# Optimization experiments

Measured on AMD Instinct MI355X. Metric: run time of the kernel, lower is better.

Reference implementation:

```python
import jax, jax.numpy as jnp
import numpy as np

B, S, D, H = 4, 1024, 1024, 16
DK = D // H
EPS = 1e-6

def setup_inputs() -> dict:
    key = jax.random.key(0)
    ks = jax.random.split(key, 7)
    scale = 1.0 / np.sqrt(D)
    return {
        "query": jax.random.normal(ks[0], (B, S, D), jnp.float32),
        "key": jax.random.normal(ks[1], (B, S, D), jnp.float32),
        "value": jax.random.normal(ks[2], (B, S, D), jnp.float32),
        "Wq": jax.random.normal(ks[3], (D, D), jnp.float32) * scale,
        "Wk": jax.random.normal(ks[4], (D, D), jnp.float32) * scale,
        "Wv": jax.random.normal(ks[5], (D, D), jnp.float32) * scale,
        "Wo": jax.random.normal(ks[6], (D, D), jnp.float32) * scale,
        "ln_gamma": jnp.ones((D,), jnp.float32),
        "ln_beta": jnp.zeros((D,), jnp.float32),
    }

def reference(query, key, value, Wq, Wk, Wv, Wo, ln_gamma, ln_beta):
    residual = query
    # projections (torch Linear: x @ W.T); reshape to [B,H,S,DK]
    def proj(x, W):
        y = jnp.einsum('bsd,ed->bse', x, W)
        return y.reshape(B, S, H, DK).transpose(0, 2, 1, 3)
    q, k, v = proj(query, Wq), proj(key, Wk), proj(value, Wv)
    scores = jnp.einsum('bhqd,bhkd->bhqk', q, k) / jnp.sqrt(jnp.float32(DK))
    p = jax.nn.softmax(scores, axis=-1)
    x = jnp.einsum('bhqk,bhkd->bhqd', p, v)
    x = x.transpose(0, 2, 1, 3).reshape(B, S, D)
    x = jnp.einsum('bsd,ed->bse', x, Wo)
    x = x + residual
    mu = jnp.mean(x, axis=-1, keepdims=True)
    var = jnp.var(x, axis=-1, keepdims=True)
    x = (x - mu) / jnp.sqrt(var + EPS) * ln_gamma + ln_beta
    return x
```

## Files before the change

kernel.cpp:

```cpp
#include <hip/hip_runtime.h>
#include <hip/hip_bf16.h>

#define B_ 4
#define S_ 1024
#define D_ 1024
#define H_ 16
#define DK_ 64
#define MROWS (B_*S_)

typedef short bf16x8 __attribute__((ext_vector_type(8)));
typedef float f32x4 __attribute__((ext_vector_type(4)));
typedef unsigned short u16;
typedef unsigned u32;
typedef u16 u16x4 __attribute__((ext_vector_type(4)));

__device__ __forceinline__ u16 f2bf(float f) {
    union { float f; unsigned u; } v; v.f = f;
    unsigned u = v.u;
    u += 0x7fff + ((u >> 16) & 1);
    return (u16)(u >> 16);
}

__device__ __forceinline__ void gld_lds16(const u16* gp, u16* lp) {
    __builtin_amdgcn_global_load_lds(
        (const __attribute__((address_space(1))) void*)gp,
        (__attribute__((address_space(3))) void*)lp,
        16, 0, 0);
}

__global__ __launch_bounds__(256) void pack_bf16(
    const float* __restrict__ q, const float* __restrict__ k, const float* __restrict__ v,
    const float* __restrict__ wq, const float* __restrict__ wk,
    const float* __restrict__ wv, const float* __restrict__ wo,
    u16* __restrict__ act_dst, u16* __restrict__ w_dst)
{
    const int NACT = 3 * MROWS * D_;
    const int NW   = 4 * D_ * D_;
    for (int c = blockIdx.x * blockDim.x + threadIdx.x;
         c < (NACT + NW) / 4; c += gridDim.x * blockDim.x) {
        int e = c * 4;
        const float* s; u16* d;
        if (e < NACT) {
            int t = e >> 22;
            int off = e & (4194304 - 1);
            s = (t == 0 ? q : t == 1 ? k : v) + off;
            d = act_dst + e;
        } else {
            int e2 = e - NACT;
            int t = e2 >> 20;
            int off = e2 & (1048576 - 1);
            s = (t == 0 ? wq : t == 1 ? wk : t == 2 ? wv : wo) + off;
            d = w_dst + e2;
        }
        float4 tv = *(const float4*)s;
        u16x4 o; o[0]=f2bf(tv.x); o[1]=f2bf(tv.y); o[2]=f2bf(tv.z); o[3]=f2bf(tv.w);
        *(u16x4*)d = o;
    }
}

template<int BM, bool EPI_RESID, bool VT>
__global__ __launch_bounds__(256) void gemm_fast(
    const u16* __restrict__ Ab, const u16* __restrict__ Wb,
    u16* __restrict__ Cb, float* __restrict__ Cf, const float* __restrict__ resid)
{
    constexpr int WN = (BM == 128) ? 2 : 4;
    constexpr int WCOLS = 128 / WN;
    constexpr int NR = WCOLS / 16;
    __shared__ u16 ldsA[BM * 64];
    __shared__ u16 ldsB[128 * 64];

    const int gx = gridDim.x, gy = gridDim.y, gz = gridDim.z;
    const int nwg = gx * gy * gz;
    const int flat = blockIdx.x + gx * (blockIdx.y + gy * blockIdx.z);
    const int f = (flat & 7) * (nwg >> 3) + (flat >> 3);
    const int bx = f % gx;
    const int rem = f / gx;
    const int by = rem % gy;
    const int z = rem / gy;

    Ab += (size_t)z * MROWS * D_;
    Wb += (size_t)z * D_ * D_;
    const u16* CbT = Cb + (EPI_RESID ? 0 : (size_t)z * MROWS * D_);
    u16* Cbz = (u16*)CbT;

    const int tid = threadIdx.x, lane = tid & 63, wid = tid >> 6;
    const int wr = (BM == 128) ? (wid >> 1) : 0;
    const int wc = (BM == 128) ? (wid & 1) : wid;
    const int m0 = by * BM, n0 = bx * 128;
    const int wbase = wid * 64;

    f32x4 acc[4][NR] = {};

    for (int kt = 0; kt < 1024; kt += 64) {
        __syncthreads();
        #pragma unroll
        for (int j = 0; j < BM / 32; ++j) {
            int ch = j * 256 + tid;
            int row = ch >> 3, c8 = (ch & 7) ^ (row & 7);
            gld_lds16(Ab + (size_t)(m0 + row) * 1024 + kt + c8 * 8,
                      &ldsA[(j * 256 + wbase) * 8]);
        }
        #pragma unroll
        for (int j = 0; j < 4; ++j) {
            int ch = j * 256 + tid;
            int row = ch >> 3, c8 = (ch & 7) ^ (row & 7);
            gld_lds16(Wb + (size_t)(n0 + row) * 1024 + kt + c8 * 8,
                      &ldsB[(j * 256 + wbase) * 8]);
        }
        __syncthreads();

        #pragma unroll
        for (int ks = 0; ks < 2; ++ks) {
            const int cb = ks * 32 + (lane >> 4) * 8;
            bf16x8 af[4], bfr[NR];
            #pragma unroll
            for (int m = 0; m < 4; ++m) {
                int row = wr * 64 + m * 16 + (lane & 15);
                af[m] = *(const bf16x8*)(&ldsA[row * 64 + (cb ^ ((row & 7) << 3))]);
            }
            #pragma unroll
            for (int n = 0; n < NR; ++n) {
                int row = wc * WCOLS + n * 16 + (lane & 15);
                bfr[n] = *(const bf16x8*)(&ldsB[row * 64 + (cb ^ ((row & 7) << 3))]);
            }
            #pragma unroll
            for (int m = 0; m < 4; ++m)
                #pragma unroll
                for (int n = 0; n < NR; ++n)
                    acc[m][n] = __builtin_amdgcn_mfma_f32_16x16x32_bf16(
                        af[m], bfr[n], acc[m][n], 0, 0, 0);
        }
    }

    if (VT && z == 2) {
        #pragma unroll
        for (int m = 0; m < 4; ++m)
            #pragma unroll
            for (int n = 0; n < NR; ++n) {
                u16x4 o;
                #pragma unroll
                for (int r = 0; r < 4; ++r) o[r] = f2bf(acc[m][n][r]);
                int grow = m0 + wr * 64 + m * 16 + (lane >> 4) * 4;
                int gcol = n0 + wc * WCOLS + n * 16 + (lane & 15);
                *(u16x4*)(&Cbz[(size_t)gcol * MROWS + grow]) = o;
            }
    } else {
        #pragma unroll
        for (int m = 0; m < 4; ++m)
            #pragma unroll
            for (int n = 0; n < NR; ++n)
                #pragma unroll
                for (int r = 0; r < 4; ++r) {
                    int grow = m0 + wr * 64 + m * 16 + (lane >> 4) * 4 + r;
                    int gcol = n0 + wc * WCOLS + n * 16 + (lane & 15);
                    if (EPI_RESID)
                        Cf[(size_t)grow * 1024 + gcol] = acc[m][n][r] + resid[(size_t)grow * 1024 + gcol];
                    else
                        Cbz[(size_t)grow * 1024 + gcol] = f2bf(acc[m][n][r]);
                }
    }
}

template<bool A_BF16, bool EPI_RESID>
__global__ __launch_bounds__(256) void gemm_bt(
    const void* __restrict__ Av, const float* __restrict__ Bw,
    u16* __restrict__ Cb, float* __restrict__ Cf,
    const float* __restrict__ resid, int M, int N, int K)
{
    __shared__ u16 lds[2][128 * 64];
    const int tid  = threadIdx.x;
    const int lane = tid & 63;
    const int wid  = tid >> 6;
    const int wr = wid >> 1, wc = wid & 1;
    const int m0 = blockIdx.y * 128, n0 = blockIdx.x * 128;

    f32x4 acc[4][4] = {};

    for (int kt = 0; kt < K; kt += 64) {
        #pragma unroll
        for (int j = 0; j < 8; ++j) {
            int idx4 = tid + 256 * j;
            int r = idx4 >> 4;
            int c = (idx4 & 15) * 4;
            u16x4 aw, bw;
            if (A_BF16) {
                const u16* Ab2 = (const u16*)Av;
                aw = *(const u16x4*)(Ab2 + (size_t)(m0 + r) * K + kt + c);
            } else {
                const float* Af = (const float*)Av;
                float4 t = *(const float4*)(Af + (size_t)(m0 + r) * K + kt + c);
                aw[0] = f2bf(t.x); aw[1] = f2bf(t.y); aw[2] = f2bf(t.z); aw[3] = f2bf(t.w);
            }
            {
                float4 t = *(const float4*)(Bw + (size_t)(n0 + r) * K + kt + c);
                bw[0] = f2bf(t.x); bw[1] = f2bf(t.y); bw[2] = f2bf(t.z); bw[3] = f2bf(t.w);
            }
            int sa = r * 64 + (c ^ ((r & 7) << 3));
            *(u16x4*)(&lds[0][sa]) = aw;
            *(u16x4*)(&lds[1][sa]) = bw;
        }
        __syncthreads();
        #pragma unroll
        for (int ks = 0; ks < 2; ++ks) {
            const int cb = ks * 32 + (lane >> 4) * 8;
            bf16x8 af[4], bfr[4];
            #pragma unroll
            for (int m = 0; m < 4; ++m) {
                int row = wr * 64 + m * 16 + (lane & 15);
                af[m] = *(const bf16x8*)(&lds[0][row * 64 + (cb ^ ((row & 7) << 3))]);
            }
            #pragma unroll
            for (int n = 0; n < 4; ++n) {
                int row = wc * 64 + n * 16 + (lane & 15);
                bfr[n] = *(const bf16x8*)(&lds[1][row * 64 + (cb ^ ((row & 7) << 3))]);
            }
            #pragma unroll
            for (int m = 0; m < 4; ++m)
                #pragma unroll
                for (int n = 0; n < 4; ++n)
                    acc[m][n] = __builtin_amdgcn_mfma_f32_16x16x32_bf16(
                        af[m], bfr[n], acc[m][n], 0, 0, 0);
        }
        __syncthreads();
    }

    #pragma unroll
    for (int m = 0; m < 4; ++m)
        #pragma unroll
        for (int n = 0; n < 4; ++n)
            #pragma unroll
            for (int r = 0; r < 4; ++r) {
                int grow = m0 + wr * 64 + m * 16 + (lane >> 4) * 4 + r;
                int gcol = n0 + wc * 64 + n * 16 + (lane & 15);
                float v = acc[m][n][r];
                if (EPI_RESID)
                    Cf[(size_t)grow * N + gcol] = v + resid[(size_t)grow * N + gcol];
                else
                    Cb[(size_t)grow * N + gcol] = f2bf(v);
            }
}

__global__ __launch_bounds__(512, 4) void attn_fwd5(
    const u16* __restrict__ Qg, const u16* __restrict__ Kg,
    const u16* __restrict__ Vt, u16* __restrict__ Og)
{
    __shared__ u16 qs[128 * 64];
    __shared__ u16 ks2[64 * 64];
    __shared__ u16 vsT[64 * 64];
    __shared__ u16 ps[128 * 64];

    const int tid = threadIdx.x, lane = tid & 63, w = tid >> 6;
    const int g = lane >> 4, ql = lane & 15;

    const int bid = blockIdx.x;
    const int f = (bid & 7) * 64 + (bid >> 3);
    const int qt = f & 7, h = (f >> 3) & 15, b = f >> 7;
    const int q0 = qt * 128;
    const size_t rbase = (size_t)b * S_;
    const int cb0 = h * DK_;

    auto stage_kv = [&](int kv0) {
        {
            int ch = tid;
            int row = ch >> 3, c8 = (ch & 7) ^ (row & 7);
            gld_lds16(Kg + (rbase + kv0 + row) * D_ + cb0 + c8 * 8, &ks2[w * 512]);
        }
        {
            int ch = tid;
            int row = ch >> 3, c8 = (ch & 7) ^ (row & 7);
            gld_lds16(Vt + (size_t)(cb0 + row) * MROWS + rbase + kv0 + c8 * 8, &vsT[w * 512]);
        }
    };

    #pragma unroll
    for (int j = 0; j < 2; ++j) {
        int idx = j * 512 + tid;
        int row = idx >> 3, c8 = (idx & 7) ^ (row & 7);
        gld_lds16(Qg + (rbase + q0 + row) * D_ + cb0 + c8 * 8,
                  &qs[(j * 512 + w * 64) * 8]);
    }
    stage_kv(0);
    __syncthreads();

    bf16x8 qb[2];
    {
        const int q = w * 16 + ql;
        #pragma unroll
        for (int ks = 0; ks < 2; ++ks) {
            int c = 32 * ks + 8 * g;
            qb[ks] = *(const bf16x8*)(&qs[q * 64 + (c ^ ((q & 7) << 3))]);
        }
    }

    float mrow = -1e30f, lrow = 0.f;
    f32x4 xacc[4] = {};

    for (int jt = 0; jt < 16; ++jt) {
        f32x4 sacc[4] = {};
        __builtin_amdgcn_s_setprio(1);
        #pragma unroll
        for (int ks = 0; ks < 2; ++ks) {
            #pragma unroll
            for (int n = 0; n < 4; ++n) {
                int krow = n * 16 + ql;
                int c = 32 * ks + 8 * g;
                bf16x8 kf = *(const bf16x8*)(&ks2[krow * 64 + (c ^ ((krow & 7) << 3))]);
                sacc[n] = __builtin_amdgcn_mfma_f32_16x16x32_bf16(kf, qb[ks], sacc[n], 0, 0, 0);
            }
        }
        __builtin_amdgcn_s_setprio(0);

        float mt = sacc[0][0];
        #pragma unroll
        for (int n = 0; n < 4; ++n)
            #pragma unroll
            for (int r = 0; r < 4; ++r) mt = fmaxf(mt, sacc[n][r]);
        mt = fmaxf(mt, __shfl_xor(mt, 16));
        mt = fmaxf(mt, __shfl_xor(mt, 32));
        float mnew = fmaxf(mrow, mt * 0.125f);
        float alpha = __expf(mrow - mnew);
        float rsum = 0.f;
        u16 pb[16];
        #pragma unroll
        for (int n = 0; n < 4; ++n)
            #pragma unroll
            for (int r = 0; r < 4; ++r) {
                float p = __expf(sacc[n][r] * 0.125f - mnew);
                rsum += p;
                pb[n * 4 + r] = f2bf(p);
            }
        rsum += __shfl_xor(rsum, 16);
        rsum += __shfl_xor(rsum, 32);
        lrow = lrow * alpha + rsum;
        mrow = mnew;

        {
            const int q = w * 16 + ql;
            #pragma unroll
            for (int n = 0; n < 4; ++n) {
                int c = 16 * n + 4 * g;
                *(u16x4*)(&ps[q * 64 + (c ^ ((q & 7) << 3))]) = *(const u16x4*)(&pb[n * 4]);
            }
        }
        asm volatile("s_waitcnt lgkmcnt(0)" ::: "memory");
        __builtin_amdgcn_sched_barrier(0);

        bf16x8 pa[2];
        {
            const int q = w * 16 + ql;
            #pragma unroll
            for (int ks = 0; ks < 2; ++ks) {
                int c = 32 * ks + 8 * g;
                pa[ks] = *(const bf16x8*)(&ps[q * 64 + (c ^ ((q & 7) << 3))]);
            }
        }
        #pragma unroll
        for (int r = 0; r < 4; ++r) {
            float a_r = __shfl(alpha, 4 * g + r);
            #pragma unroll
            for (int n2 = 0; n2 < 4; ++n2) xacc[n2][r] *= a_r;
        }

        __builtin_amdgcn_s_setprio(1);
        #pragma unroll
        for (int ks = 0; ks < 2; ++ks)
            #pragma unroll
            for (int n2 = 0; n2 < 4; ++n2) {
                int vrow = n2 * 16 + ql;
                int c2 = 32 * ks + 8 * g;
                bf16x8 bv = *(const bf16x8*)(&vsT[vrow * 64 + (c2 ^ ((vrow & 7) << 3))]);
                xacc[n2] = __builtin_amdgcn_mfma_f32_16x16x32_bf16(pa[ks], bv, xacc[n2], 0, 0, 0);
            }
        __builtin_amdgcn_s_setprio(0);

        if (jt < 15) {
            __syncthreads();
            stage_kv((jt + 1) * 64);
            __syncthreads();
        }
    }

    float linv[4];
    #pragma unroll
    for (int r = 0; r < 4; ++r) linv[r] = 1.f / __shfl(lrow, 4 * g + r);
    #pragma unroll
    for (int n2 = 0; n2 < 4; ++n2)
        #pragma unroll
        for (int r = 0; r < 4; ++r) {
            int qrow = q0 + w * 16 + 4 * g + r;
            int col = cb0 + n2 * 16 + ql;
            Og[(rbase + qrow) * D_ + col] = f2bf(xacc[n2][r] * linv[r]);
        }
}

__global__ __launch_bounds__(256) void attn_fwd(
    const u16* __restrict__ Qg, const u16* __restrict__ Kg,
    const u16* __restrict__ Vg, u16* __restrict__ Og)
{
    __shared__ u16 qs[64 * 64], ks2[64 * 64], vt[64 * 64], ps[64 * 64];
    const int tid = threadIdx.x, lane = tid & 63, w = tid >> 6;
    const int b = blockIdx.z, h = blockIdx.y, q0 = blockIdx.x * 64;
    const size_t rbase = (size_t)b * S_;
    const int cb0 = h * DK_;

    #pragma unroll
    for (int j = 0; j < 4; ++j) {
        int idx4 = tid + 256 * j;
        int r = idx4 >> 4, c = (idx4 & 15) * 4;
        u16x4 t = *(const u16x4*)(Qg + (rbase + q0 + r) * D_ + cb0 + c);
        *(u16x4*)(&qs[r * 64 + (c ^ ((r & 7) << 3))]) = t;
    }

    float mrow[4], lrow[4];
    f32x4 xacc[4] = {};
    #pragma unroll
    for (int r = 0; r < 4; ++r) { mrow[r] = -1e30f; lrow[r] = 0.f; }

    for (int jt = 0; jt < 16; ++jt) {
        const int kv0 = jt * 64;
        __syncthreads();
        #pragma unroll
        for (int j = 0; j < 4; ++j) {
            int idx4 = tid + 256 * j;
            int r = idx4 >> 4, c = (idx4 & 15) * 4;
            u16x4 t = *(const u16x4*)(Kg + (rbase + kv0 + r) * D_ + cb0 + c);
            *(u16x4*)(&ks2[r * 64 + (c ^ ((r & 7) << 3))]) = t;
            u16x4 tv = *(const u16x4*)(Vg + (rbase + kv0 + r) * D_ + cb0 + c);
            #pragma unroll
            for (int jj = 0; jj < 4; ++jj) {
                int d = c + jj;
                vt[d * 64 + (r ^ ((d & 7) << 3))] = tv[jj];
            }
        }
        __syncthreads();

        f32x4 sacc[4] = {};
        #pragma unroll
        for (int ks = 0; ks < 2; ++ks) {
            const int cb = ks * 32 + (lane >> 4) * 8;
            int qrow = w * 16 + (lane & 15);
            bf16x8 aq = *(const bf16x8*)(&qs[qrow * 64 + (cb ^ ((qrow & 7) << 3))]);
            #pragma unroll
            for (int n = 0; n < 4; ++n) {
                int krow = n * 16 + (lane & 15);
                bf16x8 bk = *(const bf16x8*)(&ks2[krow * 64 + (cb ^ ((krow & 7) << 3))]);
                sacc[n] = __builtin_amdgcn_mfma_f32_16x16x32_bf16(aq, bk, sacc[n], 0, 0, 0);
            }
        }

        #pragma unroll
        for (int r = 0; r < 4; ++r) {
            float mx = fmaxf(fmaxf(sacc[0][r], sacc[1][r]),
                             fmaxf(sacc[2][r], sacc[3][r]));
            mx = fmaxf(mx, __shfl_xor(mx, 1));
            mx = fmaxf(mx, __shfl_xor(mx, 2));
            mx = fmaxf(mx, __shfl_xor(mx, 4));
            mx = fmaxf(mx, __shfl_xor(mx, 8));
            float mnew = fmaxf(mrow[r], mx * 0.125f);
            float alpha = __expf(mrow[r] - mnew);
            float p[4], rsum = 0.f;
            #pragma unroll
            for (int n = 0; n < 4; ++n) { p[n] = __expf(sacc[n][r] * 0.125f - mnew); rsum += p[n]; }
            rsum += __shfl_xor(rsum, 1);
            rsum += __shfl_xor(rsum, 2);
            rsum += __shfl_xor(rsum, 4);
            rsum += __shfl_xor(rsum, 8);
            lrow[r] = lrow[r] * alpha + rsum;
            mrow[r] = mnew;
            int qrow = w * 16 + (lane >> 4) * 4 + r;
            #pragma unroll
            for (int n = 0; n < 4; ++n) {
                xacc[n][r] *= alpha;
                int col = n * 16 + (lane & 15);
                ps[qrow * 64 + (col ^ ((qrow & 7) << 3))] = f2bf(p[n]);
            }
        }
        __syncthreads();

        #pragma unroll
        for (int ks = 0; ks < 2; ++ks) {
            const int cb = ks * 32 + (lane >> 4) * 8;
            int prow = w * 16 + (lane & 15);
            bf16x8 ap = *(const bf16x8*)(&ps[prow * 64 + (cb ^ ((prow & 7) << 3))]);
            #pragma unroll
            for (int n = 0; n < 4; ++n) {
                int vrow = n * 16 + (lane & 15);
                bf16x8 bv = *(const bf16x8*)(&vt[vrow * 64 + (cb ^ ((vrow & 7) << 3))]);
                xacc[n] = __builtin_amdgcn_mfma_f32_16x16x32_bf16(ap, bv, xacc[n], 0, 0, 0);
            }
        }
    }

    #pragma unroll
    for (int n = 0; n < 4; ++n)
        #pragma unroll
        for (int r = 0; r < 4; ++r) {
            int qrow = q0 + w * 16 + (lane >> 4) * 4 + r;
            int col = cb0 + n * 16 + (lane & 15);
            Og[(rbase + qrow) * D_ + col] = f2bf(xacc[n][r] / lrow[r]);
        }
}

__global__ __launch_bounds__(256) void ln_inplace(
    float* __restrict__ Y, const float* __restrict__ g, const float* __restrict__ bt)
{
    __shared__ float red[2][4];
    const int row = blockIdx.x, tid = threadIdx.x;
    float4 v = *(const float4*)(Y + (size_t)row * D_ + tid * 4);
    float s = v.x + v.y + v.z + v.w;
    float q = v.x * v.x + v.y * v.y + v.z * v.z + v.w * v.w;
    #pragma unroll
    for (int m = 1; m < 64; m <<= 1) { s += __shfl_xor(s, m); q += __shfl_xor(q, m); }
    const int w = tid >> 6, lane = tid & 63;
    if (lane == 0) { red[0][w] = s; red[1][w] = q; }
    __syncthreads();
    s = red[0][0] + red[0][1] + red[0][2] + red[0][3];
    q = red[1][0] + red[1][1] + red[1][2] + red[1][3];
    float mu = s * (1.f / 1024.f);
    float var = q * (1.f / 1024.f) - mu * mu;
    float rstd = rsqrtf(var + 1e-6f);
    float4 gv = *(const float4*)(g + tid * 4);
    float4 bv = *(const float4*)(bt + tid * 4);
    v.x = (v.x - mu) * rstd * gv.x + bv.x;
    v.y = (v.y - mu) * rstd * gv.y + bv.y;
    v.z = (v.z - mu) * rstd * gv.z + bv.z;
    v.w = (v.w - mu) * rstd * gv.w + bv.w;
    *(float4*)(Y + (size_t)row * D_ + tid * 4) = v;
}

extern "C" void kernel_launch(void* const* d_in, const int* in_sizes, int n_in,
                              void* d_out, int out_size, void* d_ws, size_t ws_size,
                              hipStream_t stream)
{
    const float* query = (const float*)d_in[0];
    const float* key   = (const float*)d_in[1];
    const float* value = (const float*)d_in[2];
    const float* Wq    = (const float*)d_in[3];
    const float* Wk    = (const float*)d_in[4];
    const float* Wv    = (const float*)d_in[5];
    const float* Wo    = (const float*)d_in[6];
    const float* gamma = (const float*)d_in[7];
    const float* beta  = (const float*)d_in[8];
    float* out = (float*)d_out;

    const size_t ACT = (size_t)MROWS * D_;
    const size_t WSZ = (size_t)D_ * D_;
    const size_t NEED = (3 * ACT + 4 * WSZ + 3 * ACT) * 2;

    if (ws_size >= NEED) {
        u16* actb = (u16*)d_ws;
        u16* wb   = actb + 3 * ACT;
        u16* pb   = wb + 4 * WSZ;
        u16* Ap   = actb;

        pack_bf16<<<2048, 256, 0, stream>>>(query, key, value, Wq, Wk, Wv, Wo, actb, wb);
        gemm_fast<128, false, true><<<dim3(8, 32, 3), 256, 0, stream>>>(actb, wb, pb, nullptr, nullptr);
        attn_fwd5<<<512, 512, 0, stream>>>(pb, pb + ACT, pb + 2 * ACT, Ap);
        gemm_fast<64, true, false><<<dim3(8, 64, 1), 256, 0, stream>>>(Ap, wb + 3 * WSZ, nullptr, out, query);
        ln_inplace<<<MROWS, 256, 0, stream>>>(out, gamma, beta);
    } else {
        u16* Qp = (u16*)d_ws;
        u16* Kp = Qp + ACT;
        u16* Vp = Kp + ACT;
        u16* Ap = Vp + ACT;
        dim3 gg(D_ / 128, MROWS / 128);
        gemm_bt<false, false><<<gg, 256, 0, stream>>>(query, Wq, Qp, nullptr, nullptr, MROWS, D_, D_);
        gemm_bt<false, false><<<gg, 256, 0, stream>>>(key,   Wk, Kp, nullptr, nullptr, MROWS, D_, D_);
        gemm_bt<false, false><<<gg, 256, 0, stream>>>(value, Wv, Vp, nullptr, nullptr, MROWS, D_, D_);
        attn_fwd<<<dim3(S_ / 64, H_, B_), 256, 0, stream>>>(Qp, Kp, Vp, Ap);
        gemm_bt<true, true><<<gg, 256, 0, stream>>>(Ap, Wo, nullptr, out, query, MROWS, D_, D_);
        ln_inplace<<<MROWS, 256, 0, stream>>>(out, gamma, beta);
    }
}
```

Baseline: 122.5 us.

## Fuse fp32-to-bf16 activation conversion into QKV projection GEMM

Removes the separate pass that converted query/key/value to bf16 in a workspace. The new QKV GEMM reads fp32 activations directly, converts them in registers and writes them to swizzled LDS, while weights are still packed in advance and loaded with global_load_lds. This saves a full write and re-read of the bf16 activation copies. In exchange, the A-tile loads become synchronous register loads doubled in width, and the epilogue for Q/K uses scalar 16-bit stores, so the main loop has less overlap.

```diff
diff --git a/kernel.cpp b/kernel.cpp
--- a/kernel.cpp
+++ b/kernel.cpp
@@ -28,33 +28,125 @@
         16, 0, 0);
 }
 
-__global__ __launch_bounds__(256) void pack_bf16(
-    const float* __restrict__ q, const float* __restrict__ k, const float* __restrict__ v,
+__global__ __launch_bounds__(256) void pack_w(
     const float* __restrict__ wq, const float* __restrict__ wk,
     const float* __restrict__ wv, const float* __restrict__ wo,
-    u16* __restrict__ act_dst, u16* __restrict__ w_dst)
-{
-    const int NACT = 3 * MROWS * D_;
-    const int NW   = 4 * D_ * D_;
+    u16* __restrict__ w_dst)
+{
+    const int NW = 4 * D_ * D_;
     for (int c = blockIdx.x * blockDim.x + threadIdx.x;
-         c < (NACT + NW) / 4; c += gridDim.x * blockDim.x) {
+         c < NW / 4; c += gridDim.x * blockDim.x) {
         int e = c * 4;
-        const float* s; u16* d;
-        if (e < NACT) {
-            int t = e >> 22;
-            int off = e & (4194304 - 1);
-            s = (t == 0 ? q : t == 1 ? k : v) + off;
-            d = act_dst + e;
-        } else {
-            int e2 = e - NACT;
-            int t = e2 >> 20;
-            int off = e2 & (1048576 - 1);
-            s = (t == 0 ? wq : t == 1 ? wk : t == 2 ? wv : wo) + off;
-            d = w_dst + e2;
-        }
+        int t = e >> 20;
+        int off = e & (1048576 - 1);
+        const float* s = (t == 0 ? wq : t == 1 ? wk : t == 2 ? wv : wo) + off;
         float4 tv = *(const float4*)s;
         u16x4 o; o[0]=f2bf(tv.x); o[1]=f2bf(tv.y); o[2]=f2bf(tv.z); o[3]=f2bf(tv.w);
-        *(u16x4*)d = o;
+        *(u16x4*)(w_dst + e) = o;
+    }
+}
+
+__global__ __launch_bounds__(256) void gemm_qkv(
+    const float* __restrict__ Aq, const float* __restrict__ Ak,
+    const float* __restrict__ Avv, const u16* __restrict__ Wb,
+    u16* __restrict__ Cb)
+{
+    __shared__ u16 ldsA[128 * 64];
+    __shared__ u16 ldsB[128 * 64];
+
+    const int gx = gridDim.x, gy = gridDim.y, gz = gridDim.z;
+    const int nwg = gx * gy * gz;
+    const int flat = blockIdx.x + gx * (blockIdx.y + gy * blockIdx.z);
+    const int f = (flat & 7) * (nwg >> 3) + (flat >> 3);
+    const int bx = f % gx;
+    const int rem = f / gx;
+    const int by = rem % gy;
+    const int z = rem / gy;
+
+    const float* Af = (z == 0) ? Aq : (z == 1) ? Ak : Avv;
+    Wb += (size_t)z * D_ * D_;
+
+    const int tid = threadIdx.x, lane = tid & 63, wid = tid >> 6;
+    const int wr = wid >> 1, wc = wid & 1;
+    const int m0 = by * 128, n0 = bx * 128;
+    const int wbase = wid * 64;
+
+    f32x4 acc[4][4] = {};
+
+    for (int kt = 0; kt < 1024; kt += 64) {
+        __syncthreads();
+        #pragma unroll
+        for (int j = 0; j < 4; ++j) {
+            int g2 = j * 256 + tid;
+            int row = g2 >> 3, c8 = g2 & 7;
+            const float* src = Af + (size_t)(m0 + row) * 1024 + kt + c8 * 8;
+            float4 a0 = *(const float4*)(src);
+            float4 a1 = *(const float4*)(src + 4);
+            bf16x8 o;
+            o[0] = (short)f2bf(a0.x); o[1] = (short)f2bf(a0.y);
+            o[2] = (short)f2bf(a0.z); o[3] = (short)f2bf(a0.w);
+            o[4] = (short)f2bf(a1.x); o[5] = (short)f2bf(a1.y);
+            o[6] = (short)f2bf(a1.z); o[7] = (short)f2bf(a1.w);
+            int c8s = c8 ^ (row & 7);
+            *(bf16x8*)(&ldsA[row * 64 + c8s * 8]) = o;
+        }
+        #pragma unroll
+        for (int j = 0; j < 4; ++j) {
+            int ch = j * 256 + tid;
+            int row = ch >> 3, c8 = (ch & 7) ^ (row & 7);
+            gld_lds16(Wb + (size_t)(n0 + row) * 1024 + kt + c8 * 8,
+                      &ldsB[(j * 256 + wbase) * 8]);
+        }
+        __syncthreads();
+
+        #pragma unroll
+        for (int ks = 0; ks < 2; ++ks) {
+            const int cb = ks * 32 + (lane >> 4) * 8;
+            bf16x8 af[4], bfr[4];
+            #pragma unroll
+            for (int m = 0; m < 4; ++m) {
+                int row = wr * 64 + m * 16 + (lane & 15);
+                af[m] = *(const bf16x8*)(&ldsA[row * 64 + (cb ^ ((row & 7) << 3))]);
+            }
+            #pragma unroll
+            for (int n = 0; n < 4; ++n) {
+                int row = wc * 64 + n * 16 + (lane & 15);
+                bfr[n] = *(const bf16x8*)(&ldsB[row * 64 + (cb ^ ((row & 7) << 3))]);
+            }
+            #pragma unroll
+            for (int m = 0; m < 4; ++m)
+                #pragma unroll
+                for (int n = 0; n < 4; ++n)
+                    acc[m][n] = __builtin_amdgcn_mfma_f32_16x16x32_bf16(
+                        af[m], bfr[n], acc[m][n], 0, 0, 0);
+        }
+    }
+
+    if (z == 2) {
+        u16* Cz = Cb + 2 * (size_t)MROWS * D_;
+        #pragma unroll
+        for (int m = 0; m < 4; ++m)
+            #pragma unroll
+            for (int n = 0; n < 4; ++n) {
+                u16x4 o;
+                #pragma unroll
+                for (int r = 0; r < 4; ++r) o[r] = f2bf(acc[m][n][r]);
+                int grow = m0 + wr * 64 + m * 16 + (lane >> 4) * 4;
+                int gcol = n0 + wc * 64 + n * 16 + (lane & 15);
+                *(u16x4*)(&Cz[(size_t)gcol * MROWS + grow]) = o;
+            }
+    } else {
+        u16* Cz = Cb + (size_t)z * MROWS * D_;
+        #pragma unroll
+        for (int m = 0; m < 4; ++m)
+            #pragma unroll
+            for (int n = 0; n < 4; ++n)
+                #pragma unroll
+                for (int r = 0; r < 4; ++r) {
+                    int grow = m0 + wr * 64 + m * 16 + (lane >> 4) * 4 + r;
+                    int gcol = n0 + wc * 64 + n * 16 + (lane & 15);
+                    Cz[(size_t)grow * 1024 + gcol] = f2bf(acc[m][n][r]);
+                }
     }
 }
 
@@ -545,16 +637,15 @@
 
     const size_t ACT = (size_t)MROWS * D_;
     const size_t WSZ = (size_t)D_ * D_;
-    const size_t NEED = (3 * ACT + 4 * WSZ + 3 * ACT) * 2;
+    const size_t NEED = (4 * WSZ + 4 * ACT) * 2;
 
     if (ws_size >= NEED) {
-        u16* actb = (u16*)d_ws;
-        u16* wb   = actb + 3 * ACT;
-        u16* pb   = wb + 4 * WSZ;
-        u16* Ap   = actb;
-
-        pack_bf16<<<2048, 256, 0, stream>>>(query, key, value, Wq, Wk, Wv, Wo, actb, wb);
-        gemm_fast<128, false, true><<<dim3(8, 32, 3), 256, 0, stream>>>(actb, wb, pb, nullptr, nullptr);
+        u16* wb = (u16*)d_ws;
+        u16* pb = wb + 4 * WSZ;
+        u16* Ap = pb + 3 * ACT;
+
+        pack_w<<<1024, 256, 0, stream>>>(Wq, Wk, Wv, Wo, wb);
+        gemm_qkv<<<dim3(8, 32, 3), 256, 0, stream>>>(query, key, value, wb, pb);
         attn_fwd5<<<512, 512, 0, stream>>>(pb, pb + ACT, pb + 2 * ACT, Ap);
         gemm_fast<64, true, false><<<dim3(8, 64, 1), 256, 0, stream>>>(Ap, wb + 3 * WSZ, nullptr, out, query);
         ln_inplace<<<MROWS, 256, 0, stream>>>(out, gamma, beta);
```

Result: slower. 127.0 us (+3.7%).

## Split K/V staging across the loop, load Q to registers, and rescale lazily

Applied to the files above, without the earlier changes.

The attention kernel now loads Q straight from global memory into registers instead of staging it through LDS. It also splits the K and V prefetch so each is issued right after the last read of its buffer, which drops one barrier per iteration and overlaps the loads with softmax and PV compute. The online-softmax rescale of the accumulator, row sum and max is skipped unless some row's max grows by more than 8 in log space. This stays exact because the final division by the row sum cancels the stale max. The risk is that correctness now relies on the barriers waiting for the async LDS loads to finish, and the extra wave-vote branch adds a little overhead.

```diff
diff --git a/kernel.cpp b/kernel.cpp
--- a/kernel.cpp
+++ b/kernel.cpp
@@ -240,11 +240,10 @@
             }
 }
 
-__global__ __launch_bounds__(512, 4) void attn_fwd5(
+__global__ __launch_bounds__(512, 4) void attn_fwd6(
     const u16* __restrict__ Qg, const u16* __restrict__ Kg,
     const u16* __restrict__ Vt, u16* __restrict__ Og)
 {
-    __shared__ u16 qs[128 * 64];
     __shared__ u16 ks2[64 * 64];
     __shared__ u16 vsT[64 * 64];
     __shared__ u16 ps[128 * 64];
@@ -259,38 +258,25 @@
     const size_t rbase = (size_t)b * S_;
     const int cb0 = h * DK_;
 
-    auto stage_kv = [&](int kv0) {
-        {
-            int ch = tid;
-            int row = ch >> 3, c8 = (ch & 7) ^ (row & 7);
-            gld_lds16(Kg + (rbase + kv0 + row) * D_ + cb0 + c8 * 8, &ks2[w * 512]);
-        }
-        {
-            int ch = tid;
-            int row = ch >> 3, c8 = (ch & 7) ^ (row & 7);
-            gld_lds16(Vt + (size_t)(cb0 + row) * MROWS + rbase + kv0 + c8 * 8, &vsT[w * 512]);
-        }
-    };
-
-    #pragma unroll
-    for (int j = 0; j < 2; ++j) {
-        int idx = j * 512 + tid;
-        int row = idx >> 3, c8 = (idx & 7) ^ (row & 7);
-        gld_lds16(Qg + (rbase + q0 + row) * D_ + cb0 + c8 * 8,
-                  &qs[(j * 512 + w * 64) * 8]);
-    }
-    stage_kv(0);
-    __syncthreads();
-
     bf16x8 qb[2];
     {
-        const int q = w * 16 + ql;
-        #pragma unroll
-        for (int ks = 0; ks < 2; ++ks) {
-            int c = 32 * ks + 8 * g;
-            qb[ks] = *(const bf16x8*)(&qs[q * 64 + (c ^ ((q & 7) << 3))]);
-        }
-    }
+        const u16* qp = Qg + (rbase + q0 + w * 16 + ql) * D_ + cb0 + 8 * g;
+        qb[0] = *(const bf16x8*)(qp);
+        qb[1] = *(const bf16x8*)(qp + 32);
+    }
+
+    auto stage_k = [&](int kv0) {
+        int row = tid >> 3, c8 = (tid & 7) ^ (row & 7);
+        gld_lds16(Kg + (rbase + kv0 + row) * D_ + cb0 + c8 * 8, &ks2[w * 512]);
+    };
+    auto stage_v = [&](int kv0) {
+        int row = tid >> 3, c8 = (tid & 7) ^ (row & 7);
+        gld_lds16(Vt + (size_t)(cb0 + row) * MROWS + rbase + kv0 + c8 * 8, &vsT[w * 512]);
+    };
+
+    stage_k(0);
+    stage_v(0);
+    __syncthreads();
 
     float mrow = -1e30f, lrow = 0.f;
     f32x4 xacc[4] = {};
@@ -310,6 +296,9 @@
         }
         __builtin_amdgcn_s_setprio(0);
 
+        __syncthreads();
+        if (jt < 15) stage_k((jt + 1) * 64);
+
         float mt = sacc[0][0];
         #pragma unroll
         for (int n = 0; n < 4; ++n)
@@ -317,22 +306,31 @@
             for (int r = 0; r < 4; ++r) mt = fmaxf(mt, sacc[n][r]);
         mt = fmaxf(mt, __shfl_xor(mt, 16));
         mt = fmaxf(mt, __shfl_xor(mt, 32));
-        float mnew = fmaxf(mrow, mt * 0.125f);
-        float alpha = __expf(mrow - mnew);
+        if (!__all(mt * 0.125f - mrow <= 8.f)) {
+            float mnew = fmaxf(mrow, mt * 0.125f);
+            float alpha = __expf(mrow - mnew);
+            mrow = mnew;
+            lrow *= alpha;
+            #pragma unroll
+            for (int r = 0; r < 4; ++r) {
+                float a_r = __shfl(alpha, 4 * g + r);
+                #pragma unroll
+                for (int n2 = 0; n2 < 4; ++n2) xacc[n2][r] *= a_r;
+            }
+        }
         float rsum = 0.f;
         u16 pb[16];
         #pragma unroll
         for (int n = 0; n < 4; ++n)
             #pragma unroll
             for (int r = 0; r < 4; ++r) {
-                float p = __expf(sacc[n][r] * 0.125f - mnew);
+                float p = __expf(sacc[n][r] * 0.125f - mrow);
                 rsum += p;
                 pb[n * 4 + r] = f2bf(p);
             }
         rsum += __shfl_xor(rsum, 16);
         rsum += __shfl_xor(rsum, 32);
-        lrow = lrow * alpha + rsum;
-        mrow = mnew;
+        lrow += rsum;
 
         {
             const int q = w * 16 + ql;
@@ -353,12 +351,6 @@
                 int c = 32 * ks + 8 * g;
                 pa[ks] = *(const bf16x8*)(&ps[q * 64 + (c ^ ((q & 7) << 3))]);
             }
-        }
-        #pragma unroll
-        for (int r = 0; r < 4; ++r) {
-            float a_r = __shfl(alpha, 4 * g + r);
-            #pragma unroll
-            for (int n2 = 0; n2 < 4; ++n2) xacc[n2][r] *= a_r;
         }
 
         __builtin_amdgcn_s_setprio(1);
@@ -373,11 +365,8 @@
             }
         __builtin_amdgcn_s_setprio(0);
 
-        if (jt < 15) {
-            __syncthreads();
-            stage_kv((jt + 1) * 64);
-            __syncthreads();
-        }
+        __syncthreads();
+        if (jt < 15) stage_v((jt + 1) * 64);
     }
 
     float linv[4];
@@ -555,7 +544,7 @@
 
         pack_bf16<<<2048, 256, 0, stream>>>(query, key, value, Wq, Wk, Wv, Wo, actb, wb);
         gemm_fast<128, false, true><<<dim3(8, 32, 3), 256, 0, stream>>>(actb, wb, pb, nullptr, nullptr);
-        attn_fwd5<<<512, 512, 0, stream>>>(pb, pb + ACT, pb + 2 * ACT, Ap);
+        attn_fwd6<<<512, 512, 0, stream>>>(pb, pb + ACT, pb + 2 * ACT, Ap);
         gemm_fast<64, true, false><<<dim3(8, 64, 1), 256, 0, stream>>>(Ap, wb + 3 * WSZ, nullptr, out, query);
         ln_inplace<<<MROWS, 256, 0, stream>>>(out, gamma, beta);
     } else {
```

Measured after the change: 119.6 us. 2.4% less time.
